# Optimization experiments

Measured on AMD Instinct MI355X. Metric: run time of the kernel, lower is better.

The kernel has to match this reference:

```python
import jax, jax.numpy as jnp
import numpy as np

B, N, C, H = 4, 1024, 768, 12
HD = C // H

def setup_inputs() -> dict:
    key = jax.random.key(0)
    ks = jax.random.split(key, 6)
    s = 0.02
    return {
        "x": jax.random.normal(ks[0], (B, N, C), jnp.float32),
        "attn_bias": jax.random.normal(ks[1], (H, N, N), jnp.float32),
        "qkv_w": jax.random.normal(ks[2], (C, 3 * C), jnp.float32) * s,
        "qkv_b": jax.random.normal(ks[3], (3 * C,), jnp.float32) * s,
        "proj_w": jax.random.normal(ks[4], (C, C), jnp.float32) * s,
        "proj_b": jax.random.normal(ks[5], (C,), jnp.float32) * s,
    }

def reference(x, attn_bias, qkv_w, qkv_b, proj_w, proj_b):
    b, n, c = x.shape
    scale = HD ** -0.5
    qkv = x @ qkv_w + qkv_b                      # [B,N,3C]
    qkv = qkv.reshape(b, n, 3, H, HD)
    q = qkv[:, :, 0].transpose(0, 2, 1, 3)       # [B,H,N,HD]
    k = qkv[:, :, 1].transpose(0, 2, 1, 3)
    v = qkv[:, :, 2].transpose(0, 2, 1, 3)
    attn = jnp.einsum('bhqd,bhkd->bhqk', q, k) * scale
    attn = attn + attn_bias[None]                # broadcast over batch
    attn = jax.nn.softmax(attn, axis=-1)
    y = jnp.einsum('bhqk,bhkd->bhqd', attn, v)   # [B,H,N,HD]
    y = y.transpose(0, 2, 1, 3).reshape(b, n, c)
    return y @ proj_w + proj_b
```

## Files before the change

### kernel.cpp

```cpp
#include <hip/hip_runtime.h>
#include <hip/hip_bf16.h>

constexpr int BATCH = 4;
constexpr int NSEQ  = 1024;
constexpr int CDIM  = 768;
constexpr int NHEAD = 12;
constexpr int HDIM  = 64;
constexpr int MTOT  = BATCH * NSEQ;
constexpr int QKVN  = 3 * CDIM;

typedef __bf16 bf16x8 __attribute__((ext_vector_type(8)));
typedef float  f32x4  __attribute__((ext_vector_type(4)));

__device__ __forceinline__ unsigned short f2bf(float f) {
    unsigned u = __builtin_bit_cast(unsigned, f);
    unsigned r = u + 0x7FFFu + ((u >> 16) & 1u);
    return (unsigned short)(r >> 16);
}

#define GLOAD_LDS16(gp, lp)                                                    \
    __builtin_amdgcn_global_load_lds(                                          \
        (const __attribute__((address_space(1))) void*)(gp),                   \
        (__attribute__((address_space(3))) void*)(lp), 16, 0, 0)

__global__ __launch_bounds__(256) void cvt_f32_bf16(
    const float* __restrict__ in, unsigned short* __restrict__ out, int n4)
{
    int i = blockIdx.x * 256 + threadIdx.x;
    if (i < n4) {
        float4 a = reinterpret_cast<const float4*>(in)[i];
        ushort4 h;
        h.x = f2bf(a.x); h.y = f2bf(a.y); h.z = f2bf(a.z); h.w = f2bf(a.w);
        reinterpret_cast<ushort4*>(out)[i] = h;
    }
}

__global__ __launch_bounds__(256) void tcvt_f32_bf16(
    const float* __restrict__ in, unsigned short* __restrict__ out, int R, int C)
{
    __shared__ unsigned short t[32][33];
    const int c0 = blockIdx.x * 32, r0 = blockIdx.y * 32;
    const int tc = threadIdx.x & 31, tr = threadIdx.x >> 5;
    #pragma unroll
    for (int i = 0; i < 4; i++)
        t[tc][tr + 8 * i] = f2bf(in[(size_t)(r0 + tr + 8 * i) * C + c0 + tc]);
    __syncthreads();
    #pragma unroll
    for (int i = 0; i < 4; i++)
        out[(size_t)(c0 + tr + 8 * i) * R + r0 + tc] = t[tr + 8 * i][tc];
}

__global__ __launch_bounds__(256) void qkv_gemm(
    const unsigned short* __restrict__ xb,
    const unsigned short* __restrict__ wt,
    const float* __restrict__ bias,
    unsigned short* __restrict__ qbuf, unsigned short* __restrict__ kbuf,
    unsigned short* __restrict__ vtbuf)
{
    __shared__ unsigned short As[128 * 32];
    __shared__ unsigned short Bs[128 * 32];
    const int tid  = threadIdx.x;
    const int lane = tid & 63;
    const int wid  = tid >> 6;
    const int wm = (wid >> 1) * 64, wn = (wid & 1) * 64;
    const int g = lane >> 4, li = lane & 15;
    const int m0 = blockIdx.y * 128;
    const int n0 = blockIdx.x * 128;
    const int srow = lane >> 2;
    const int scol = (lane & 3) * 8;

    f32x4 acc[4][4];
    #pragma unroll
    for (int i = 0; i < 4; i++)
        #pragma unroll
        for (int j = 0; j < 4; j++) acc[i][j] = f32x4{0.f, 0.f, 0.f, 0.f};

    for (int k0 = 0; k0 < CDIM; k0 += 32) {
        __syncthreads();
        #pragma unroll
        for (int c = 0; c < 2; c++) {
            int row = wid * 32 + c * 16 + srow;
            GLOAD_LDS16(&xb[(size_t)(m0 + row) * CDIM + k0 + scol],
                        &As[(wid * 32 + c * 16) * 32]);
            GLOAD_LDS16(&wt[(size_t)(n0 + row) * CDIM + k0 + scol],
                        &Bs[(wid * 32 + c * 16) * 32]);
        }
        __syncthreads();
        bf16x8 a[4], b[4];
        #pragma unroll
        for (int mt = 0; mt < 4; mt++)
            a[mt] = *reinterpret_cast<const bf16x8*>(&As[(wm + 16 * mt + li) * 32 + 8 * g]);
        #pragma unroll
        for (int nt = 0; nt < 4; nt++)
            b[nt] = *reinterpret_cast<const bf16x8*>(&Bs[(wn + 16 * nt + li) * 32 + 8 * g]);
        #pragma unroll
        for (int mt = 0; mt < 4; mt++)
            #pragma unroll
            for (int nt = 0; nt < 4; nt++)
                acc[mt][nt] = __builtin_amdgcn_mfma_f32_16x16x32_bf16(a[mt], b[nt], acc[mt][nt], 0, 0, 0);
    }

    #pragma unroll
    for (int mt = 0; mt < 4; mt++) {
        #pragma unroll
        for (int nt = 0; nt < 4; nt++) {
            int col  = n0 + wn + 16 * nt + li;
            int tsel = col / CDIM;
            int rem  = col - tsel * CDIM;
            int h_ = rem >> 6, d = rem & 63;
            float bv = bias[col];
            float sc = (tsel == 0) ? 0.125f : 1.0f;
            #pragma unroll
            for (int r = 0; r < 4; r++) {
                int m  = m0 + wm + 16 * mt + 4 * g + r;
                int b_ = m >> 10, s = m & 1023;
                unsigned short hv = f2bf((acc[mt][nt][r] + bv) * sc);
                if (tsel == 0)
                    qbuf[(((size_t)b_ * NHEAD + h_) * NSEQ + s) * HDIM + d] = hv;
                else if (tsel == 1)
                    kbuf[(((size_t)b_ * NHEAD + h_) * NSEQ + s) * HDIM + d] = hv;
                else
                    vtbuf[(((size_t)b_ * NHEAD + h_) * HDIM + d) * NSEQ + s] = hv;
            }
        }
    }
}

__global__ __launch_bounds__(256, 4) void attn_kernel(
    const unsigned short* __restrict__ qbuf,
    const unsigned short* __restrict__ kbuf,
    const unsigned short* __restrict__ vtbuf,
    const float* __restrict__ bias,
    unsigned short* __restrict__ ybuf)
{
    __shared__ unsigned short Kl[2][64 * 64];
    __shared__ unsigned short Vl[2][64 * 64];
    __shared__ unsigned short Ps[4 * 16 * 64];

    const int tid  = threadIdx.x;
    const int lane = tid & 63;
    const int wid  = tid >> 6;
    const int g = lane >> 4, li = lane & 15;
    const int srow8 = lane >> 3;
    const int scs   = (lane & 7) ^ srow8;
    const int bh = blockIdx.y;
    const int b_ = bh / NHEAD, h_ = bh % NHEAD;
    const int qw = blockIdx.x * 64 + wid * 16;

    const unsigned short* qb = qbuf + (size_t)bh * NSEQ * HDIM;
    const unsigned short* kb = kbuf + (size_t)bh * NSEQ * HDIM;
    const unsigned short* vb = vtbuf + (size_t)bh * HDIM * NSEQ;
    const float* bb = bias + (size_t)h_ * NSEQ * NSEQ;

#define STAGE_KV(T, KL, VL)                                                    \
    {                                                                          \
        _Pragma("unroll") for (int i = 0; i < 2; i++) {                        \
            GLOAD_LDS16(kb + (size_t)((T) * 64 + wid * 16 + i * 8 + srow8) * HDIM + scs * 8, \
                        (KL) + (wid * 16 + i * 8) * 64);                       \
            GLOAD_LDS16(vb + (size_t)(wid * 16 + i * 8 + srow8) * NSEQ + (T) * 64 + scs * 8, \
                        (VL) + (wid * 16 + i * 8) * 64);                       \
        }                                                                      \
    }

#define COMPUTE_TILE(KS, VS, T)                                                \
    {                                                                          \
        float bv[4][4];                                                        \
        _Pragma("unroll") for (int kt = 0; kt < 4; kt++)                       \
            _Pragma("unroll") for (int r = 0; r < 4; r++)                      \
                bv[kt][r] = bb[(size_t)(qw + 4 * g + r) * NSEQ + (T) * 64 + 16 * kt + li]; \
        f32x4 sacc[4];                                                         \
        _Pragma("unroll") for (int kt = 0; kt < 4; kt++)                       \
            sacc[kt] = f32x4{0.f, 0.f, 0.f, 0.f};                              \
        _Pragma("unroll") for (int kt = 0; kt < 4; kt++)                       \
            _Pragma("unroll") for (int dd = 0; dd < 2; dd++) {                 \
                bf16x8 kf = *reinterpret_cast<const bf16x8*>(                  \
                    (KS) + (16 * kt + li) * 64 + (((4 * dd + g) ^ (li & 7)) * 8)); \
                sacc[kt] = __builtin_amdgcn_mfma_f32_16x16x32_bf16(qf[dd], kf, sacc[kt], 0, 0, 0); \
            }                                                                  \
        _Pragma("unroll") for (int kt = 0; kt < 4; kt++)                       \
            _Pragma("unroll") for (int r = 0; r < 4; r++) {                    \
                float pv = __expf(sacc[kt][r] + bv[kt][r]);                    \
                lpart[r] += pv;                                                \
                Ps[wid * 1024 + (4 * g + r) * 64 +                             \
                   (((2 * kt + (li >> 3)) ^ ((4 * g + r) & 7)) * 8) + (li & 7)] = f2bf(pv); \
            }                                                                  \
        _Pragma("unroll") for (int kk = 0; kk < 2; kk++) {                     \
            bf16x8 pf = *reinterpret_cast<const bf16x8*>(                      \
                &Ps[wid * 1024 + li * 64 + (((4 * kk + g) ^ (li & 7)) * 8)]);  \
            _Pragma("unroll") for (int dt = 0; dt < 4; dt++) {                 \
                bf16x8 vf = *reinterpret_cast<const bf16x8*>(                  \
                    (VS) + (16 * dt + li) * 64 + (((4 * kk + g) ^ (li & 7)) * 8)); \
                oacc[dt] = __builtin_amdgcn_mfma_f32_16x16x32_bf16(pf, vf, oacc[dt], 0, 0, 0); \
            }                                                                  \
        }                                                                      \
    }

    bf16x8 qf[2];
    #pragma unroll
    for (int dd = 0; dd < 2; dd++)
        qf[dd] = *reinterpret_cast<const bf16x8*>(&qb[(size_t)(qw + li) * HDIM + 32 * dd + 8 * g]);

    f32x4 oacc[4];
    #pragma unroll
    for (int dt = 0; dt < 4; dt++) oacc[dt] = f32x4{0.f, 0.f, 0.f, 0.f};
    float lpart[4] = {0.f, 0.f, 0.f, 0.f};

    STAGE_KV(0, Kl[0], Vl[0]);
    __syncthreads();

    for (int j = 0; j < 8; ++j) {
        const int tA = 2 * j;
        STAGE_KV(tA + 1, Kl[1], Vl[1]);
        COMPUTE_TILE(Kl[0], Vl[0], tA);
        __syncthreads();

        if (j < 7) STAGE_KV(tA + 2, Kl[0], Vl[0]);
        COMPUTE_TILE(Kl[1], Vl[1], tA + 1);
        __syncthreads();
    }

    float linv[4];
    #pragma unroll
    for (int r = 0; r < 4; r++) {
        float s = lpart[r];
        s += __shfl_xor(s, 1);
        s += __shfl_xor(s, 2);
        s += __shfl_xor(s, 4);
        s += __shfl_xor(s, 8);
        linv[r] = 1.f / s;
    }
    #pragma unroll
    for (int dt = 0; dt < 4; dt++)
        #pragma unroll
        for (int r = 0; r < 4; r++) {
            float o = oacc[dt][r] * linv[r];
            int sq = qw + 4 * g + r;
            ybuf[((size_t)b_ * NSEQ + sq) * CDIM + h_ * HDIM + 16 * dt + li] = f2bf(o);
        }
#undef STAGE_KV
#undef COMPUTE_TILE
}

__global__ __launch_bounds__(256) void proj_gemm(
    const unsigned short* __restrict__ yb,
    const unsigned short* __restrict__ pwt,
    const float* __restrict__ bias, float* __restrict__ out)
{
    __shared__ unsigned short As[128 * 32];
    __shared__ unsigned short Bs[128 * 32];
    const int tid  = threadIdx.x;
    const int lane = tid & 63;
    const int wid  = tid >> 6;
    const int wm = (wid >> 1) * 64, wn = (wid & 1) * 64;
    const int g = lane >> 4, li = lane & 15;
    const int m0 = blockIdx.y * 128;
    const int n0 = blockIdx.x * 128;
    const int srow = lane >> 2;
    const int scol = (lane & 3) * 8;

    f32x4 acc[4][4];
    #pragma unroll
    for (int i = 0; i < 4; i++)
        #pragma unroll
        for (int j = 0; j < 4; j++) acc[i][j] = f32x4{0.f, 0.f, 0.f, 0.f};

    for (int k0 = 0; k0 < CDIM; k0 += 32) {
        __syncthreads();
        #pragma unroll
        for (int c = 0; c < 2; c++) {
            int row = wid * 32 + c * 16 + srow;
            GLOAD_LDS16(&yb[(size_t)(m0 + row) * CDIM + k0 + scol],
                        &As[(wid * 32 + c * 16) * 32]);
            GLOAD_LDS16(&pwt[(size_t)(n0 + row) * CDIM + k0 + scol],
                        &Bs[(wid * 32 + c * 16) * 32]);
        }
        __syncthreads();
        bf16x8 a[4], b[4];
        #pragma unroll
        for (int mt = 0; mt < 4; mt++)
            a[mt] = *reinterpret_cast<const bf16x8*>(&As[(wm + 16 * mt + li) * 32 + 8 * g]);
        #pragma unroll
        for (int nt = 0; nt < 4; nt++)
            b[nt] = *reinterpret_cast<const bf16x8*>(&Bs[(wn + 16 * nt + li) * 32 + 8 * g]);
        #pragma unroll
        for (int mt = 0; mt < 4; mt++)
            #pragma unroll
            for (int nt = 0; nt < 4; nt++)
                acc[mt][nt] = __builtin_amdgcn_mfma_f32_16x16x32_bf16(a[mt], b[nt], acc[mt][nt], 0, 0, 0);
    }

    #pragma unroll
    for (int mt = 0; mt < 4; mt++)
        #pragma unroll
        for (int nt = 0; nt < 4; nt++) {
            int col = n0 + wn + 16 * nt + li;
            float bv = bias[col];
            #pragma unroll
            for (int r = 0; r < 4; r++) {
                int m = m0 + wm + 16 * mt + 4 * g + r;
                out[(size_t)m * CDIM + col] = acc[mt][nt][r] + bv;
            }
        }
}

extern "C" void kernel_launch(void* const* d_in, const int* in_sizes, int n_in,
                              void* d_out, int out_size, void* d_ws, size_t ws_size,
                              hipStream_t stream) {
    const float* x         = (const float*)d_in[0];
    const float* attn_bias = (const float*)d_in[1];
    const float* qkv_w     = (const float*)d_in[2];
    const float* qkv_b     = (const float*)d_in[3];
    const float* proj_w    = (const float*)d_in[4];
    const float* proj_b    = (const float*)d_in[5];
    float* out = (float*)d_out;

    const size_t per = (size_t)BATCH * NHEAD * NSEQ * HDIM;
    unsigned short* qbuf  = (unsigned short*)d_ws;
    unsigned short* kbuf  = qbuf + per;
    unsigned short* vtbuf = kbuf + per;
    unsigned short* xb    = vtbuf + per;
    unsigned short* qwt   = xb + per;
    unsigned short* pwt   = qwt + (size_t)QKVN * CDIM;
    unsigned short* ybuf  = xb;

    cvt_f32_bf16<<<(MTOT * CDIM / 4 + 255) / 256, 256, 0, stream>>>(
        x, xb, MTOT * CDIM / 4);
    tcvt_f32_bf16<<<dim3(QKVN / 32, CDIM / 32), 256, 0, stream>>>(
        qkv_w, qwt, CDIM, QKVN);
    tcvt_f32_bf16<<<dim3(CDIM / 32, CDIM / 32), 256, 0, stream>>>(
        proj_w, pwt, CDIM, CDIM);

    qkv_gemm<<<dim3(QKVN / 128, MTOT / 128), 256, 0, stream>>>(
        xb, qwt, qkv_b, qbuf, kbuf, vtbuf);
    attn_kernel<<<dim3(NSEQ / 64, BATCH * NHEAD), 256, 0, stream>>>(
        qbuf, kbuf, vtbuf, attn_bias, ybuf);
    proj_gemm<<<dim3(CDIM / 128, MTOT / 128), 256, 0, stream>>>(
        ybuf, pwt, proj_b, out);
}
```

Baseline: 107.4 us.

## Stage attention bias through LDS via async loads and shrink KV tile to 32

The attention kernel now brings the fp32 bias tile into shared memory with async global-to-LDS loads, double-buffered alongside K and V, instead of each lane reading bias straight from global memory inside the compute loop. To fit the extra bias buffer, the key tile drops from 64 to 32, which doubles the loop trip count. The P scratch gets a padded layout in place of the XOR swizzle. The aim is to hide bias-load latency behind MFMA work, at the cost of more barriers per key and less work per iteration.

```diff
diff --git a/kernel.cpp b/kernel.cpp
--- a/kernel.cpp
+++ b/kernel.cpp
@@ -133,65 +133,70 @@
     const float* __restrict__ bias,
     unsigned short* __restrict__ ybuf)
 {
-    __shared__ unsigned short Kl[2][64 * 64];
-    __shared__ unsigned short Vl[2][64 * 64];
-    __shared__ unsigned short Ps[4 * 16 * 64];
+    __shared__ unsigned short Kl[2][32 * 64];
+    __shared__ unsigned short Vl[2][64 * 32];
+    __shared__ float          Bl[2][64 * 32];
+    __shared__ unsigned short Ps[4 * 16 * 40];
 
     const int tid  = threadIdx.x;
     const int lane = tid & 63;
     const int wid  = tid >> 6;
     const int g = lane >> 4, li = lane & 15;
     const int srow8 = lane >> 3;
-    const int scs   = (lane & 7) ^ srow8;
+    const int scs8  = (lane & 7) ^ srow8;
+    const int vrow4 = lane >> 2;
+    const int scs4  = (lane & 3) ^ (vrow4 & 3);
     const int bh = blockIdx.y;
     const int b_ = bh / NHEAD, h_ = bh % NHEAD;
-    const int qw = blockIdx.x * 64 + wid * 16;
+    const int qblk = blockIdx.x * 64;
+    const int qw = qblk + wid * 16;
 
     const unsigned short* qb = qbuf + (size_t)bh * NSEQ * HDIM;
     const unsigned short* kb = kbuf + (size_t)bh * NSEQ * HDIM;
     const unsigned short* vb = vtbuf + (size_t)bh * HDIM * NSEQ;
-    const float* bb = bias + (size_t)h_ * NSEQ * NSEQ;
-
-#define STAGE_KV(T, KL, VL)                                                    \
+    const float* bbq = bias + (size_t)h_ * NSEQ * NSEQ + (size_t)qblk * NSEQ;
+
+#define STAGE(T, KL, VL, BL)                                                   \
     {                                                                          \
-        _Pragma("unroll") for (int i = 0; i < 2; i++) {                        \
-            GLOAD_LDS16(kb + (size_t)((T) * 64 + wid * 16 + i * 8 + srow8) * HDIM + scs * 8, \
-                        (KL) + (wid * 16 + i * 8) * 64);                       \
-            GLOAD_LDS16(vb + (size_t)(wid * 16 + i * 8 + srow8) * NSEQ + (T) * 64 + scs * 8, \
-                        (VL) + (wid * 16 + i * 8) * 64);                       \
+        GLOAD_LDS16(kb + (size_t)((T) * 32 + wid * 8 + srow8) * HDIM + scs8 * 8, \
+                    (KL) + wid * 8 * 64);                                      \
+        GLOAD_LDS16(vb + (size_t)(wid * 16 + vrow4) * NSEQ + (T) * 32 + scs4 * 8, \
+                    (VL) + wid * 16 * 32);                                     \
+        GLOAD_LDS16(bbq + (size_t)(wid * 16 + srow8) * NSEQ + (T) * 32 + scs8 * 4, \
+                    (BL) + (wid * 16) * 32);                                   \
+        GLOAD_LDS16(bbq + (size_t)(wid * 16 + 8 + srow8) * NSEQ + (T) * 32 + scs8 * 4, \
+                    (BL) + (wid * 16 + 8) * 32);                               \
+    }
+
+#define COMPUTE(KS, VS, BS)                                                    \
+    {                                                                          \
+        f32x4 s0 = f32x4{0.f, 0.f, 0.f, 0.f};                                  \
+        f32x4 s1 = f32x4{0.f, 0.f, 0.f, 0.f};                                  \
+        _Pragma("unroll") for (int dd = 0; dd < 2; dd++) {                     \
+            bf16x8 kf0 = *reinterpret_cast<const bf16x8*>(                     \
+                (KS) + li * 64 + (((4 * dd + g) ^ (li & 7)) * 8));             \
+            bf16x8 kf1 = *reinterpret_cast<const bf16x8*>(                     \
+                (KS) + (16 + li) * 64 + (((4 * dd + g) ^ (li & 7)) * 8));      \
+            s0 = __builtin_amdgcn_mfma_f32_16x16x32_bf16(qf[dd], kf0, s0, 0, 0, 0); \
+            s1 = __builtin_amdgcn_mfma_f32_16x16x32_bf16(qf[dd], kf1, s1, 0, 0, 0); \
         }                                                                      \
-    }
-
-#define COMPUTE_TILE(KS, VS, T)                                                \
-    {                                                                          \
-        float bv[4][4];                                                        \
-        _Pragma("unroll") for (int kt = 0; kt < 4; kt++)                       \
-            _Pragma("unroll") for (int r = 0; r < 4; r++)                      \
-                bv[kt][r] = bb[(size_t)(qw + 4 * g + r) * NSEQ + (T) * 64 + 16 * kt + li]; \
-        f32x4 sacc[4];                                                         \
-        _Pragma("unroll") for (int kt = 0; kt < 4; kt++)                       \
-            sacc[kt] = f32x4{0.f, 0.f, 0.f, 0.f};                              \
-        _Pragma("unroll") for (int kt = 0; kt < 4; kt++)                       \
-            _Pragma("unroll") for (int dd = 0; dd < 2; dd++) {                 \
-                bf16x8 kf = *reinterpret_cast<const bf16x8*>(                  \
-                    (KS) + (16 * kt + li) * 64 + (((4 * dd + g) ^ (li & 7)) * 8)); \
-                sacc[kt] = __builtin_amdgcn_mfma_f32_16x16x32_bf16(qf[dd], kf, sacc[kt], 0, 0, 0); \
-            }                                                                  \
-        _Pragma("unroll") for (int kt = 0; kt < 4; kt++)                       \
-            _Pragma("unroll") for (int r = 0; r < 4; r++) {                    \
-                float pv = __expf(sacc[kt][r] + bv[kt][r]);                    \
-                lpart[r] += pv;                                                \
-                Ps[wid * 1024 + (4 * g + r) * 64 +                             \
-                   (((2 * kt + (li >> 3)) ^ ((4 * g + r) & 7)) * 8) + (li & 7)] = f2bf(pv); \
-            }                                                                  \
-        _Pragma("unroll") for (int kk = 0; kk < 2; kk++) {                     \
-            bf16x8 pf = *reinterpret_cast<const bf16x8*>(                      \
-                &Ps[wid * 1024 + li * 64 + (((4 * kk + g) ^ (li & 7)) * 8)]);  \
-            _Pragma("unroll") for (int dt = 0; dt < 4; dt++) {                 \
-                bf16x8 vf = *reinterpret_cast<const bf16x8*>(                  \
-                    (VS) + (16 * dt + li) * 64 + (((4 * kk + g) ^ (li & 7)) * 8)); \
-                oacc[dt] = __builtin_amdgcn_mfma_f32_16x16x32_bf16(pf, vf, oacc[dt], 0, 0, 0); \
-            }                                                                  \
+        _Pragma("unroll") for (int r = 0; r < 4; r++) {                        \
+            int row = 4 * g + r;                                               \
+            float b0 = (BS)[(wid * 16 + row) * 32 +                            \
+                            (((li >> 2) ^ (row & 7)) * 4) + (li & 3)];         \
+            float b1 = (BS)[(wid * 16 + row) * 32 +                            \
+                            (((4 + (li >> 2)) ^ (row & 7)) * 4) + (li & 3)];   \
+            float p0 = __expf(s0[r] + b0);                                     \
+            float p1 = __expf(s1[r] + b1);                                     \
+            lpart[r] += p0 + p1;                                               \
+            Ps[wid * 640 + row * 40 + li]      = f2bf(p0);                     \
+            Ps[wid * 640 + row * 40 + 16 + li] = f2bf(p1);                     \
+        }                                                                      \
+        bf16x8 pf = *reinterpret_cast<const bf16x8*>(&Ps[wid * 640 + li * 40 + 8 * g]); \
+        _Pragma("unroll") for (int dt = 0; dt < 4; dt++) {                     \
+            bf16x8 vf = *reinterpret_cast<const bf16x8*>(                      \
+                (VS) + (16 * dt + li) * 32 + ((g ^ (li & 3)) * 8));            \
+            oacc[dt] = __builtin_amdgcn_mfma_f32_16x16x32_bf16(pf, vf, oacc[dt], 0, 0, 0); \
         }                                                                      \
     }
 
@@ -205,17 +210,17 @@
     for (int dt = 0; dt < 4; dt++) oacc[dt] = f32x4{0.f, 0.f, 0.f, 0.f};
     float lpart[4] = {0.f, 0.f, 0.f, 0.f};
 
-    STAGE_KV(0, Kl[0], Vl[0]);
+    STAGE(0, Kl[0], Vl[0], Bl[0]);
     __syncthreads();
 
-    for (int j = 0; j < 8; ++j) {
+    for (int j = 0; j < 16; ++j) {
         const int tA = 2 * j;
-        STAGE_KV(tA + 1, Kl[1], Vl[1]);
-        COMPUTE_TILE(Kl[0], Vl[0], tA);
-        __syncthreads();
-
-        if (j < 7) STAGE_KV(tA + 2, Kl[0], Vl[0]);
-        COMPUTE_TILE(Kl[1], Vl[1], tA + 1);
+        STAGE(tA + 1, Kl[1], Vl[1], Bl[1]);
+        COMPUTE(Kl[0], Vl[0], Bl[0]);
+        __syncthreads();
+
+        if (j < 15) STAGE(tA + 2, Kl[0], Vl[0], Bl[0]);
+        COMPUTE(Kl[1], Vl[1], Bl[1]);
         __syncthreads();
     }
 
@@ -237,8 +242,8 @@
             int sq = qw + 4 * g + r;
             ybuf[((size_t)b_ * NSEQ + sq) * CDIM + h_ * HDIM + 16 * dt + li] = f2bf(o);
         }
-#undef STAGE_KV
-#undef COMPUTE_TILE
+#undef STAGE
+#undef COMPUTE
 }
 
 __global__ __launch_bounds__(256) void proj_gemm(
```

Result: slower. 116.0 us (+8.0%).
